# Kernel optimization log

Hardware: AMD Instinct MI355X
Metric: run time of the kernel (lower is better)

The kernel has to match this reference:

```python
import jax, jax.numpy as jnp
import numpy as np
import math

N_HEADS = 64
N_KV_HEADS = 8
HEAD_DIM = 128
DIM = 8192
SEQLEN = 2048
KVLEN = 2048
BSZ = 1


def setup_inputs() -> dict:
    key = jax.random.key(0)
    k1, k2, k3, k4, k5 = jax.random.split(key, 5)
    xq = jax.random.normal(k1, (SEQLEN, N_HEADS, BSZ, HEAD_DIM), dtype=jnp.float32)
    keys = jax.random.normal(k2, (BSZ, N_KV_HEADS, KVLEN, HEAD_DIM), dtype=jnp.float32)
    values = jax.random.normal(k3, (BSZ, N_KV_HEADS, KVLEN, HEAD_DIM), dtype=jnp.float32)
    attn_mask = jax.random.normal(k4, (SEQLEN, 1, 1, KVLEN), dtype=jnp.float32)
    wo_w = jax.random.normal(k5, (DIM, DIM), dtype=jnp.float32) * (1.0 / math.sqrt(DIM))
    return {"xq": xq, "keys": keys, "values": values, "attn_mask": attn_mask, "wo_w": wo_w}


def reference(xq, keys, values, attn_mask, wo_w):
    n_rep = N_HEADS // N_KV_HEADS
    bsz = xq.shape[2]
    seqlen = xq.shape[0]
    # repeat_kv: expand kv heads to n_heads (torch expand+reshape == jnp.repeat on head axis)
    k = jnp.repeat(keys, n_rep, axis=1)    # (b, n_heads, kv, d)
    v = jnp.repeat(values, n_rep, axis=1)  # (b, n_heads, kv, d)
    q = jnp.transpose(xq, (2, 1, 0, 3))    # (b, n_heads, s, d)
    mask = jnp.transpose(attn_mask, (2, 1, 0, 3))  # (b_or_1, h_or_1, s, kv)
    scores = jnp.einsum('bhsd,bhtd->bhst', q, k) / math.sqrt(HEAD_DIM)
    scores = scores + mask
    probs = jax.nn.softmax(scores.astype(jnp.float32), axis=-1).astype(q.dtype)
    out = jnp.einsum('bhst,bhtd->bhsd', probs, v)  # (b, h, s, d)
    out = jnp.transpose(out, (0, 2, 1, 3)).reshape(bsz, seqlen, -1)  # (b, s, h*d)
    return out @ wo_w.T  # Linear wo, no bias
```

## Files before the change

kernel.cpp:

```cpp
#include <hip/hip_runtime.h>
#include <hip/hip_bf16.h>
#include <stdint.h>


typedef __bf16 bf16;
typedef __attribute__((ext_vector_type(8))) __bf16 bf16x8;
typedef __attribute__((ext_vector_type(4))) __bf16 bf16x4;
typedef __attribute__((ext_vector_type(4))) float f32x4;
typedef __attribute__((ext_vector_type(16))) float f32x16;
typedef __attribute__((ext_vector_type(4))) unsigned int u32x4;

#define N_HEADS 64
#define N_KVH   8
#define HDIM    128
#define SEQ     2048
#define KVL     2048
#define DIM     8192

__device__ __forceinline__ void gload16(const void* g, void* l) {
  __builtin_amdgcn_global_load_lds((const __attribute__((address_space(1))) void*)g,
                                   (__attribute__((address_space(3))) void*)l,
                                   16, 0, 0);
}

__device__ __forceinline__ unsigned pack2(float lo, float hi) {
  union { bf16 h; unsigned short u; } a, b;
  a.h = (bf16)lo; b.h = (bf16)hi;
  return ((unsigned)b.u << 16) | (unsigned)a.u;
}

__device__ __forceinline__ void exch(unsigned a, unsigned b, unsigned& r0, unsigned& r1) {
  asm("v_permlane32_swap_b32 %0, %1" : "+v"(a), "+v"(b));
  r0 = a; r1 = b;
}

__device__ __forceinline__ void buildfrags(const float (&p)[16], bf16x8& f0, bf16x8& f1) {
  unsigned pk0 = pack2(p[0],  p[1]),  pk1 = pack2(p[2],  p[3]);
  unsigned pk2 = pack2(p[4],  p[5]),  pk3 = pack2(p[6],  p[7]);
  unsigned pk4 = pack2(p[8],  p[9]),  pk5 = pack2(p[10], p[11]);
  unsigned pk6 = pack2(p[12], p[13]), pk7 = pack2(p[14], p[15]);
  unsigned a0, a1, b0, b1, c0, c1, d0, d1;
  exch(pk0, pk2, a0, a1);
  exch(pk1, pk3, b0, b1);
  exch(pk4, pk6, c0, c1);
  exch(pk5, pk7, d0, d1);
  u32x4 w0 = { a0, b0, a1, b1 };
  u32x4 w1 = { c0, d0, c1, d1 };
  f0 = __builtin_bit_cast(bf16x8, w0);
  f1 = __builtin_bit_cast(bf16x8, w1);
}

#define WO_F4  16777216l
#define XQ_F4   4194304l
#define K_F4     524288l
__global__ void cvt_all(const float* __restrict__ wo, const float* __restrict__ xq,
                        const float* __restrict__ ks,
                        bf16* __restrict__ woB, bf16* __restrict__ qB,
                        bf16* __restrict__ kB) {
  long i = (long)blockIdx.x * blockDim.x + threadIdx.x;
  const long stride = (long)gridDim.x * blockDim.x;
  const long total = WO_F4 + XQ_F4 + K_F4;
  for (; i < total; i += stride) {
    const float* src; bf16* dst; float sc; long j;
    if (i < WO_F4)              { src = wo; dst = woB; sc = 1.0f; j = i; }
    else if (i < WO_F4 + XQ_F4) { src = xq; dst = qB;  sc = 0.08838834764831845f; j = i - WO_F4; }
    else                        { src = ks; dst = kB;  sc = 1.0f; j = i - WO_F4 - XQ_F4; }
    float4 v = ((const float4*)src)[j];
    bf16x4 o = { (bf16)(v.x * sc), (bf16)(v.y * sc),
                 (bf16)(v.z * sc), (bf16)(v.w * sc) };
    *(bf16x4*)(dst + j * 4) = o;
  }
}

__global__ void cvt_vT_kernel(const float* __restrict__ v, bf16* __restrict__ vT) {
  __shared__ bf16 tile[64][132];
  const int tid = threadIdx.x;
  const int kh = blockIdx.x >> 5;
  const int t0 = (blockIdx.x & 31) << 6;
  const float* src = v + ((long)kh * KVL + t0) * HDIM;
#pragma unroll
  for (int it = 0; it < 8; ++it) {
    int q = it * 256 + tid;
    int r = q >> 5;
    int c4 = (q & 31) << 2;
    float4 val = *(const float4*)(src + (long)r * HDIM + c4);
    bf16x4 o = { (bf16)val.x, (bf16)val.y, (bf16)val.z, (bf16)val.w };
    *(bf16x4*)&tile[r][c4] = o;
  }
  __syncthreads();
  const int t = tid & 63;
  const int dbase = tid >> 6;
#pragma unroll
  for (int it = 0; it < 32; ++it) {
    int d = it * 4 + dbase;
    vT[((long)kh * HDIM + d) * KVL + t0 + t] = tile[t][d];
  }
}

__global__ __launch_bounds__(256, 2) void attn_kernel(
    const bf16* __restrict__ qB, const bf16* __restrict__ kB,
    const bf16* __restrict__ vT, const float* __restrict__ mask,
    bf16* __restrict__ attnB)
{
  __shared__ __align__(16) char lds[65536];

  const int tid  = threadIdx.x;
  const int lane = tid & 63;
  const int w    = tid >> 6;
  const int ihi  = lane >> 5;
  const int l31  = lane & 31;

  const int bid = blockIdx.x;
  const int h   = bid >> 4;
  const int q0b = (bid & 15) << 7;
  const int kh  = h >> 3;

#pragma unroll
  for (int rnd = 0; rnd < 8; ++rnd) {
    int row = rnd * 16 + w * 4 + (lane >> 4);
    int cg  = (lane & 15) ^ (row & 15);
    const bf16* g = qB + (((long)(q0b + row) * N_HEADS + h) << 7) + (cg << 3);
    gload16(g, lds + rnd * 4096 + w * 1024);
  }
  __syncthreads();

  bf16x8 qf[8];
  {
    int qrow = (w << 5) + l31;
    const char* qr = lds + qrow * 256;
#pragma unroll
    for (int s = 0; s < 8; ++s)
      qf[s] = *(const bf16x8*)(qr + ((((s << 1) | ihi) ^ (qrow & 15)) << 4));
  }
  __syncthreads();

  {
#pragma unroll
    for (int rnd = 0; rnd < 4; ++rnd) {
      int row = rnd * 16 + w * 4 + (lane >> 4);
      int cg  = (lane & 15) ^ (row & 15);
      const bf16* g = kB + (((long)(kh * KVL + row)) << 7) + (cg << 3);
      gload16(g, lds + rnd * 4096 + w * 1024);
    }
#pragma unroll
    for (int rnd = 0; rnd < 4; ++rnd) {
      int vr = rnd * 16 + w * 4 + (lane >> 4);
      int gg = (lane & 15) ^ (vr & 15);
      int dsrc = (vr << 1) | (gg >> 3);
      const bf16* gp = vT + ((long)(kh * HDIM + dsrc) * KVL) + ((gg & 7) << 3);
      gload16(gp, lds + 32768 + rnd * 4096 + w * 1024);
    }
  }
  __syncthreads();

  const float* mrow = mask + (size_t)(q0b + (w << 5) + l31) * KVL + (ihi << 2);

  f32x16 acc[4];
#pragma unroll
  for (int dt = 0; dt < 4; ++dt) acc[dt] = {};
  float m_run = -1e30f, l_run = 0.f;

  for (int kt = 0; kt < KVL / 64; ++kt) {
    const int cur = kt & 1;
    const int kv0 = kt << 6;

    if (kt < KVL / 64 - 1) {
      const int kv0n = kv0 + 64;
#pragma unroll
      for (int rnd = 0; rnd < 4; ++rnd) {
        int row = rnd * 16 + w * 4 + (lane >> 4);
        int cg  = (lane & 15) ^ (row & 15);
        const bf16* g = kB + (((long)(kh * KVL + kv0n + row)) << 7) + (cg << 3);
        gload16(g, lds + (cur ^ 1) * 16384 + rnd * 4096 + w * 1024);
      }
#pragma unroll
      for (int rnd = 0; rnd < 4; ++rnd) {
        int vr = rnd * 16 + w * 4 + (lane >> 4);
        int gg = (lane & 15) ^ (vr & 15);
        int dsrc = (vr << 1) | (gg >> 3);
        const bf16* gp = vT + ((long)(kh * HDIM + dsrc) * KVL) + kv0n + ((gg & 7) << 3);
        gload16(gp, lds + 32768 + (cur ^ 1) * 16384 + rnd * 4096 + w * 1024);
      }
    }

    const float* mrt = mrow + kv0;
    f32x4 mk0[4], mk1[4];
#pragma unroll
    for (int rq = 0; rq < 4; ++rq) {
      mk0[rq] = *(const f32x4*)(mrt + (rq << 3));
      mk1[rq] = *(const f32x4*)(mrt + 32 + (rq << 3));
    }

    const char* kb = lds + cur * 16384;
    f32x16 s0 = {}, s1 = {};
    const int kr0 = l31, kr1 = 32 + l31;
    __builtin_amdgcn_s_setprio(1);
#pragma unroll
    for (int s = 0; s < 8; ++s) {
      bf16x8 kf0 = *(const bf16x8*)(kb + kr0 * 256 + ((((s << 1) | ihi) ^ (kr0 & 15)) << 4));
      s0 = __builtin_amdgcn_mfma_f32_32x32x16_bf16(kf0, qf[s], s0, 0, 0, 0);
      bf16x8 kf1 = *(const bf16x8*)(kb + kr1 * 256 + ((((s << 1) | ihi) ^ (kr1 & 15)) << 4));
      s1 = __builtin_amdgcn_mfma_f32_32x32x16_bf16(kf1, qf[s], s1, 0, 0, 0);
    }
    __builtin_amdgcn_s_setprio(0);

    float p0[16], p1[16];
#pragma unroll
    for (int rq = 0; rq < 4; ++rq) {
#pragma unroll
      for (int j = 0; j < 4; ++j) {
        p0[rq * 4 + j] = s0[rq * 4 + j] + mk0[rq][j];
        p1[rq * 4 + j] = s1[rq * 4 + j] + mk1[rq][j];
      }
    }

    float q00 = fmaxf(fmaxf(p0[0],  p0[1]),  fmaxf(p0[2],  p0[3]));
    float q01 = fmaxf(fmaxf(p0[4],  p0[5]),  fmaxf(p0[6],  p0[7]));
    float q02 = fmaxf(fmaxf(p0[8],  p0[9]),  fmaxf(p0[10], p0[11]));
    float q03 = fmaxf(fmaxf(p0[12], p0[13]), fmaxf(p0[14], p0[15]));
    float q10 = fmaxf(fmaxf(p1[0],  p1[1]),  fmaxf(p1[2],  p1[3]));
    float q11 = fmaxf(fmaxf(p1[4],  p1[5]),  fmaxf(p1[6],  p1[7]));
    float q12 = fmaxf(fmaxf(p1[8],  p1[9]),  fmaxf(p1[10], p1[11]));
    float q13 = fmaxf(fmaxf(p1[12], p1[13]), fmaxf(p1[14], p1[15]));
    float mx = fmaxf(fmaxf(fmaxf(q00, q01), fmaxf(q02, q03)),
                     fmaxf(fmaxf(q10, q11), fmaxf(q12, q13)));
    mx = fmaxf(mx, __shfl_xor(mx, 32));
    if (!__all((int)(mx - m_run <= 8.0f))) {
      float nm = fmaxf(m_run, mx);
      float al = __expf(m_run - nm);
      m_run = nm;
      l_run *= al;
#pragma unroll
      for (int dt = 0; dt < 4; ++dt) acc[dt] *= al;
    }
    float ps = 0.f;
#pragma unroll
    for (int i = 0; i < 16; ++i) { p0[i] = __expf(p0[i] - m_run); ps += p0[i]; }
#pragma unroll
    for (int i = 0; i < 16; ++i) { p1[i] = __expf(p1[i] - m_run); ps += p1[i]; }
    ps += __shfl_xor(ps, 32);
    l_run += ps;

    bf16x8 pfrag[4];
    buildfrags(p0, pfrag[0], pfrag[1]);
    buildfrags(p1, pfrag[2], pfrag[3]);

    const char* vb = lds + 32768 + cur * 16384;
    const int par8 = (l31 & 1) << 3;
    __builtin_amdgcn_s_setprio(1);
#pragma unroll
    for (int dt = 0; dt < 4; ++dt) {
      const int vrow = (dt << 4) + (l31 >> 1);
      const char* vrp = vb + vrow * 256;
#pragma unroll
      for (int ks = 0; ks < 4; ++ks) {
        int c16 = par8 | (ks << 1) | ihi;
        bf16x8 vf = *(const bf16x8*)(vrp + ((c16 ^ (vrow & 15)) << 4));
        acc[dt] = __builtin_amdgcn_mfma_f32_32x32x16_bf16(vf, pfrag[ks], acc[dt], 0, 0, 0);
      }
    }
    __builtin_amdgcn_s_setprio(0);
    __syncthreads();
  }

  const float linv = 1.0f / l_run;
  char* ep = lds + (w << 13);
#pragma unroll
  for (int dt = 0; dt < 4; ++dt) {
#pragma unroll
    for (int r = 0; r < 16; ++r) {
      int d = (dt << 5) + (r & 3) + ((r >> 2) << 3) + (ihi << 2);
      int byte = l31 * 256 + (((d >> 3) ^ (l31 & 15)) << 4) + ((d & 7) << 1);
      *(bf16*)(ep + byte) = (bf16)(acc[dt][r] * linv);
    }
  }
  __syncthreads();
  const size_t obase = (size_t)(q0b + (w << 5)) * DIM + h * HDIM;
#pragma unroll
  for (int i = 0; i < 8; ++i) {
    int row = (i << 2) + (lane >> 4);
    int cp  = lane & 15;
    int c   = cp ^ (row & 15);
    bf16x8 ov = *(const bf16x8*)(ep + row * 256 + (cp << 4));
    *(bf16x8*)(attnB + obase + (size_t)row * DIM + (c << 3)) = ov;
  }
}

__global__ __launch_bounds__(512, 2) void gemm_bt(
    const bf16* __restrict__ A, const bf16* __restrict__ B, float* __restrict__ C)
{
  __shared__ __align__(16) char lds[131072];
  const int tid  = threadIdx.x;
  const int lane = tid & 63;
  const int w    = tid >> 6;
  const int wm   = w >> 2;
  const int wn   = w & 3;

  const int bid = blockIdx.x;
  const int m0  = (bid >> 5) << 8;
  const int n0  = (((bid & 7) << 2) | ((bid >> 3) & 3)) << 8;

  const int srow = tid >> 3;
  const int sch  = (tid & 7) ^ (srow & 7);
  const bf16* gA0 = A + (long)(m0 + srow) * DIM + (sch << 3);
  const bf16* gB0 = B + (long)(n0 + srow) * DIM + (sch << 3);
  const long rstep = (long)64 * DIM;

  f32x4 acc[8][4];
#pragma unroll
  for (int i = 0; i < 8; ++i)
#pragma unroll
    for (int j = 0; j < 4; ++j) acc[i][j] = { 0.f, 0.f, 0.f, 0.f };

  auto STAGE = [&](int kt) {
    const long ko = (long)kt << 6;
    char* s = lds + (kt & 1) * 65536 + tid * 16;
#pragma unroll
    for (int l = 0; l < 4; ++l)
      gload16(gA0 + l * rstep + ko, s + l * 8192);
#pragma unroll
    for (int l = 0; l < 4; ++l)
      gload16(gB0 + l * rstep + ko, s + 32768 + l * 8192);
  };

  const int g = lane >> 4;
  const int l15 = lane & 15;
  auto COMPUTE = [&](int buf) {
    const char* ab = lds + buf * 65536;
    const char* bb = ab + 32768;
    bf16x8 bfr[4][2];
#pragma unroll
    for (int j = 0; j < 4; ++j) {
      int n = (wn << 6) + (j << 4) + l15;
      const char* nr = bb + n * 128;
#pragma unroll
      for (int ks = 0; ks < 2; ++ks)
        bfr[j][ks] = *(const bf16x8*)(nr + ((((ks << 2) | g) ^ (n & 7)) << 4));
    }
#pragma unroll
    for (int p = 0; p < 4; ++p) {
      bf16x8 af[2][2];
#pragma unroll
      for (int e = 0; e < 2; ++e) {
        int m = (wm << 7) + (((p << 1) | e) << 4) + l15;
        const char* mr = ab + m * 128;
#pragma unroll
        for (int ks = 0; ks < 2; ++ks)
          af[e][ks] = *(const bf16x8*)(mr + ((((ks << 2) | g) ^ (m & 7)) << 4));
      }
      __builtin_amdgcn_s_setprio(1);
#pragma unroll
      for (int e = 0; e < 2; ++e)
#pragma unroll
        for (int j = 0; j < 4; ++j)
#pragma unroll
          for (int ks = 0; ks < 2; ++ks)
            acc[(p << 1) | e][j] =
              __builtin_amdgcn_mfma_f32_16x16x32_bf16(af[e][ks], bfr[j][ks],
                                                      acc[(p << 1) | e][j], 0, 0, 0);
      __builtin_amdgcn_s_setprio(0);
    }
  };

  STAGE(0);
  STAGE(1);

  for (int t = 0; t < 126; ++t) {
    asm volatile("s_waitcnt vmcnt(8)" ::: "memory");
    __builtin_amdgcn_s_barrier();
    COMPUTE(t & 1);
    __builtin_amdgcn_s_barrier();
    STAGE(t + 2);
  }
  asm volatile("s_waitcnt vmcnt(8)" ::: "memory");
  __builtin_amdgcn_s_barrier();
  COMPUTE(0);
  asm volatile("s_waitcnt vmcnt(0)" ::: "memory");
  __builtin_amdgcn_s_barrier();
  COMPUTE(1);

#pragma unroll
  for (int i = 0; i < 8; ++i) {
#pragma unroll
    for (int rr = 0; rr < 4; ++rr) {
      float* cp = C + (long)(m0 + (wm << 7) + (i << 4) + ((lane >> 4) << 2) + rr) * DIM
                    + n0 + (wn << 6) + l15;
#pragma unroll
      for (int j = 0; j < 4; ++j)
        cp[j * 16] = acc[i][j][rr];
    }
  }
}

extern "C" void kernel_launch(void* const* d_in, const int* in_sizes, int n_in,
                              void* d_out, int out_size, void* d_ws, size_t ws_size,
                              hipStream_t stream) {
  const float* xq     = (const float*)d_in[0];
  const float* keys   = (const float*)d_in[1];
  const float* values = (const float*)d_in[2];
  const float* mask   = (const float*)d_in[3];
  const float* wo     = (const float*)d_in[4];
  float* out = (float*)d_out;
  char* ws = (char*)d_ws;

  bf16* woB = (bf16*)ws;
  bf16* qB  = (bf16*)(ws + 134217728ull);
  bf16* kB  = (bf16*)(ws + 134217728ull + 33554432ull);
  bf16* vT  = (bf16*)(ws + 134217728ull + 37748736ull);
  bf16* aB  = (bf16*)(ws + 134217728ull + 41943040ull);

  cvt_all<<<dim3(2560), dim3(256), 0, stream>>>(wo, xq, keys, woB, qB, kB);
  cvt_vT_kernel<<<dim3(256), dim3(256), 0, stream>>>(values, vT);
  attn_kernel<<<dim3(1024),  dim3(256), 0, stream>>>(qB, kB, vT, mask, aB);
  gemm_bt<<<dim3(256),       dim3(512), 0, stream>>>(aB, woB, out);
}
```

Baseline: 523.4 us.

## Interleave global-to-LDS tile loads with MFMA phases in output projection GEMM

The wo GEMM main loop no longer issues all eight global-to-LDS loads for tile t+2 in one burst after compute. Loads are now split per row-chunk and spread across the four MFMA sub-phases, with barriers between sub-phases. Each chunk is written only after the warps that read it are done, and two A chunks are deferred to the next iteration. The aim is to overlap memory traffic with matrix math and smooth issue pressure. The cost is more barriers per iteration and a fragile vmcnt accounting scheme.

```diff
diff --git a/kernel.cpp b/kernel.cpp
--- a/kernel.cpp
+++ b/kernel.cpp
@@ -312,22 +312,41 @@
 #pragma unroll
     for (int j = 0; j < 4; ++j) acc[i][j] = { 0.f, 0.f, 0.f, 0.f };
 
-  auto STAGE = [&](int kt) {
+  auto stageA = [&](int kt, int l) {
     const long ko = (long)kt << 6;
     char* s = lds + (kt & 1) * 65536 + tid * 16;
-#pragma unroll
-    for (int l = 0; l < 4; ++l)
-      gload16(gA0 + l * rstep + ko, s + l * 8192);
-#pragma unroll
-    for (int l = 0; l < 4; ++l)
-      gload16(gB0 + l * rstep + ko, s + 32768 + l * 8192);
+    gload16(gA0 + l * rstep + ko, s + l * 8192);
+  };
+  auto stageB = [&](int kt, int l) {
+    const long ko = (long)kt << 6;
+    char* s = lds + (kt & 1) * 65536 + 32768 + tid * 16;
+    gload16(gB0 + l * rstep + ko, s + l * 8192);
   };
 
   const int g = lane >> 4;
   const int l15 = lane & 15;
-  auto COMPUTE = [&](int buf) {
-    const char* ab = lds + buf * 65536;
+
+  for (int t = 0; t < 128; ++t) {
+    const char* ab = lds + (t & 1) * 65536;
     const char* bb = ab + 32768;
+
+    if (t == 0) {
+#pragma unroll
+      for (int l = 0; l < 4; ++l) { stageA(0, l); }
+#pragma unroll
+      for (int l = 0; l < 4; ++l) { stageB(0, l); }
+#pragma unroll
+      for (int l = 0; l < 4; ++l) { stageA(1, l); }
+#pragma unroll
+      for (int l = 0; l < 4; ++l) { stageB(1, l); }
+      asm volatile("s_waitcnt vmcnt(8)" ::: "memory");
+    } else if (t == 127) {
+      asm volatile("s_waitcnt vmcnt(0)" ::: "memory");
+    } else {
+      asm volatile("s_waitcnt vmcnt(6)" ::: "memory");
+    }
+    __builtin_amdgcn_s_barrier();
+
     bf16x8 bfr[4][2];
 #pragma unroll
     for (int j = 0; j < 4; ++j) {
@@ -337,8 +356,32 @@
       for (int ks = 0; ks < 2; ++ks)
         bfr[j][ks] = *(const bf16x8*)(nr + ((((ks << 2) | g) ^ (n & 7)) << 4));
     }
-#pragma unroll
-    for (int p = 0; p < 4; ++p) {
+    {
+      bf16x8 af[2][2];
+#pragma unroll
+      for (int e = 0; e < 2; ++e) {
+        int m = (wm << 7) + (e << 4) + l15;
+        const char* mr = ab + m * 128;
+#pragma unroll
+        for (int ks = 0; ks < 2; ++ks)
+          af[e][ks] = *(const bf16x8*)(mr + ((((ks << 2) | g) ^ (m & 7)) << 4));
+      }
+      if (t >= 1 && t <= 126) { stageA(t + 1, 1); stageA(t + 1, 3); }
+      __builtin_amdgcn_s_setprio(1);
+#pragma unroll
+      for (int e = 0; e < 2; ++e)
+#pragma unroll
+        for (int j = 0; j < 4; ++j)
+#pragma unroll
+          for (int ks = 0; ks < 2; ++ks)
+            acc[e][j] = __builtin_amdgcn_mfma_f32_16x16x32_bf16(
+                af[e][ks], bfr[j][ks], acc[e][j], 0, 0, 0);
+      __builtin_amdgcn_s_setprio(0);
+    }
+
+#pragma unroll
+    for (int p = 1; p < 4; ++p) {
+      __builtin_amdgcn_s_barrier();
       bf16x8 af[2][2];
 #pragma unroll
       for (int e = 0; e < 2; ++e) {
@@ -348,6 +391,11 @@
         for (int ks = 0; ks < 2; ++ks)
           af[e][ks] = *(const bf16x8*)(mr + ((((ks << 2) | g) ^ (m & 7)) << 4));
       }
+      if (t + 2 < 128) {
+        if (p == 1)      { stageB(t + 2, 0); stageB(t + 2, 1); }
+        else if (p == 2) { stageB(t + 2, 2); stageB(t + 2, 3); stageA(t + 2, 0); }
+        else             { stageA(t + 2, 2); }
+      }
       __builtin_amdgcn_s_setprio(1);
 #pragma unroll
       for (int e = 0; e < 2; ++e)
@@ -355,29 +403,12 @@
         for (int j = 0; j < 4; ++j)
 #pragma unroll
           for (int ks = 0; ks < 2; ++ks)
-            acc[(p << 1) | e][j] =
-              __builtin_amdgcn_mfma_f32_16x16x32_bf16(af[e][ks], bfr[j][ks],
-                                                      acc[(p << 1) | e][j], 0, 0, 0);
+            acc[(p << 1) | e][j] = __builtin_amdgcn_mfma_f32_16x16x32_bf16(
+                af[e][ks], bfr[j][ks], acc[(p << 1) | e][j], 0, 0, 0);
       __builtin_amdgcn_s_setprio(0);
     }
-  };
-
-  STAGE(0);
-  STAGE(1);
-
-  for (int t = 0; t < 126; ++t) {
-    asm volatile("s_waitcnt vmcnt(8)" ::: "memory");
     __builtin_amdgcn_s_barrier();
-    COMPUTE(t & 1);
-    __builtin_amdgcn_s_barrier();
-    STAGE(t + 2);
-  }
-  asm volatile("s_waitcnt vmcnt(8)" ::: "memory");
-  __builtin_amdgcn_s_barrier();
-  COMPUTE(0);
-  asm volatile("s_waitcnt vmcnt(0)" ::: "memory");
-  __builtin_amdgcn_s_barrier();
-  COMPUTE(1);
+  }
 
 #pragma unroll
   for (int i = 0; i < 8; ++i) {
```

After: 515.0 us. No clear change (-1.6%).
